# Optimization experiments

Measured on AMD Instinct MI355X. Metric: run time of the kernel, lower is better.

## Reference

```python
import jax, jax.numpy as jnp
import numpy as np

B, S, D, H = 8, 2048, 1024, 16
HD = D // H          # head_dim = 64
HID = 4 * HD         # hidden = 256
MAX_LR = 0.01
NUM_LAYERS = 2


def _split_heads(x):
    b, s, _ = x.shape
    return x.reshape(b, s, H, HD).transpose(0, 2, 1, 3).reshape(b * H, s, HD)


def _merge_heads(x, b):
    return x.reshape(b, H, -1, HD).transpose(0, 2, 1, 3).reshape(b, -1, D)


def _rmsnorm_w(x, w, eps=1e-6):
    # learned RMSNorm: x / rms(x) * w
    return x * w * jax.lax.rsqrt(jnp.mean(x * x, axis=-1, keepdims=True) + eps)


def _pf_rmsnorm(h):
    # parameter-free RMSNorm, returns (h_norm, rms)
    rms = jnp.sqrt(jnp.mean(h * h, axis=-1, keepdims=True) + 1e-8)
    return h / rms, rms


def _pf_rmsnorm_bwd(d_out, h_norm, rms):
    d = d_out.shape[-1]
    dy = jnp.sum(d_out * h_norm, axis=-1, keepdims=True)
    return (d_out - h_norm * dy / d) / rms


def _gelu_grad(x):
    cdf = 0.5 * (1.0 + jax.lax.erf(x * 0.7071067811865476))
    pdf = jnp.exp(-0.5 * x * x) * 0.3989422804014327
    return cdf + x * pdf


def _memory_forward(x, Ws):
    h = x
    n = len(Ws)
    for i, W in enumerate(Ws):
        h = jnp.matmul(h, W)  # (BH,S,din) @ (BH,din,dout)
        if i < n - 1:
            h = jax.nn.gelu(h, approximate=False)
    h = jnp.nan_to_num(h, nan=0.0, posinf=0.0, neginf=0.0)
    h_norm, _ = _pf_rmsnorm(h)
    return h_norm + x


def _memory_grad(keys, values, theta, Ws):
    Ws = [jax.lax.stop_gradient(W) for W in Ws]  # detach fast weights
    acts = [keys]
    pres = []
    h = keys
    n = len(Ws)
    for i, W in enumerate(Ws):
        pre = jnp.matmul(h, W)
        pres.append(pre)
        h = jax.nn.gelu(pre, approximate=False) if i < n - 1 else pre
        acts.append(h)
    h_norm, rms = _pf_rmsnorm(acts[-1])
    pred = h_norm + keys
    d_pred = 2.0 * theta[..., None] * (pred - values)
    d_h = _pf_rmsnorm_bwd(d_pred, h_norm, rms)
    grads = [None] * n
    for i in range(n - 1, -1, -1):
        grads[i] = jnp.einsum('bsi,bso->bio', acts[i], d_h)
        if i > 0:
            d_h = jnp.matmul(d_h, Ws[i].transpose(0, 2, 1)) * _gelu_grad(pres[i - 1])
    return grads


def _clip_grads(grads, max_norm=10.0):
    sq = sum(jnp.sum(g.reshape(g.shape[0], -1) ** 2, axis=1) for g in grads)
    coef = jnp.minimum(max_norm / (jnp.sqrt(sq) + 1e-6), 1.0)
    coef = jax.lax.stop_gradient(coef)[:, None, None]
    return [g * coef for g in grads]


def reference(x, W_K, W_V, W_Q, mem_W0, mem_W1, k_norm_w, q_norm_w,
              store_norm_w, retrieve_norm_w, alpha_w, alpha_b,
              theta_w, theta_b, eta_w, eta_b):
    b = x.shape[0]
    bh = b * H
    # init per-sample fast weights and zero momentum
    Ws = [jnp.broadcast_to(mem_W0, (bh,) + mem_W0.shape),
          jnp.broadcast_to(mem_W1, (bh,) + mem_W1.shape)]
    mom = [jnp.zeros_like(W) for W in Ws]
    # ---- update(x, ms, mom) ----
    x_n = _rmsnorm_w(x, store_norm_w)
    keys = _rmsnorm_w(_split_heads(x_n @ W_K), k_norm_w)
    values = _split_heads(x_n @ W_V)
    alpha = jax.nn.sigmoid(x_n @ alpha_w + alpha_b)          # (B,S,H)
    theta = jax.nn.sigmoid(x_n @ theta_w + theta_b) * MAX_LR
    eta = jax.nn.sigmoid(x_n @ eta_w + eta_b)
    to_bh = lambda t: t.transpose(0, 2, 1).reshape(bh, -1)   # (BH,S)
    alpha, theta, eta = to_bh(alpha), to_bh(theta), to_bh(eta)
    grads = _clip_grads(_memory_grad(keys, values, theta, Ws))
    a_mean = jnp.mean(alpha, axis=1)[:, None, None]
    e_mean = jnp.mean(eta, axis=1)[:, None, None]
    new_Ws = []
    for W, m, g in zip(Ws, mom, grads):
        new_m = e_mean * m - g
        new_w = (1.0 - a_mean) * W + new_m
        new_w = jnp.where(jnp.isfinite(new_w), new_w, jax.lax.stop_gradient(W))
        new_Ws.append(new_w)
    # ---- retrieve(x, new_ms) ----
    q = _rmsnorm_w(_split_heads(_rmsnorm_w(x, retrieve_norm_w) @ W_Q), q_norm_w)
    out = _memory_forward(q, new_Ws)
    return _merge_heads(out, b)


def setup_inputs() -> dict:
    key = jax.random.key(0)
    ks = jax.random.split(key, 12)
    xav0 = float(np.sqrt(2.0 / (HD + HID)))
    xav1 = float(np.sqrt(2.0 / (HID + HD)))
    return {
        'x': jax.random.normal(ks[0], (B, S, D), jnp.float32),
        'W_K': jax.random.normal(ks[1], (D, D), jnp.float32) / np.float32(np.sqrt(D)),
        'W_V': jax.random.normal(ks[2], (D, D), jnp.float32) / np.float32(np.sqrt(D)),
        'W_Q': jax.random.normal(ks[3], (D, D), jnp.float32) / np.float32(np.sqrt(D)),
        'mem_W0': jax.random.normal(ks[4], (HD, HID), jnp.float32) * xav0,
        'mem_W1': jax.random.normal(ks[5], (HID, HD), jnp.float32) * xav1,
        'k_norm_w': jnp.ones((HD,), jnp.float32),
        'q_norm_w': jnp.ones((HD,), jnp.float32),
        'store_norm_w': jnp.ones((D,), jnp.float32),
        'retrieve_norm_w': jnp.ones((D,), jnp.float32),
        'alpha_w': jax.random.normal(ks[6], (D, H), jnp.float32) * 0.01,
        'alpha_b': jnp.full((H,), -5.0, jnp.float32),
        'theta_w': jax.random.normal(ks[7], (D, H), jnp.float32) * 0.01,
        'theta_b': jnp.full((H,), -3.0, jnp.float32),
        'eta_w': jax.random.normal(ks[8], (D, H), jnp.float32) * 0.01,
        'eta_b': jnp.zeros((H,), jnp.float32),
    }
```

## Files before the change

### kernel.cpp

```cpp
#include <hip/hip_runtime.h>

typedef unsigned short u16;
typedef unsigned int   u32;

#define DEV static __device__ __forceinline__

constexpr int S    = 2048;
constexpr int D    = 1024;
constexpr int H    = 16;
constexpr int BB   = 8;
constexpr int BH   = BB * H;
constexpr int BS   = BB * S;
constexpr long NR  = (long)BH * S;
constexpr int GB   = 16;
constexpr int NG   = BH / GB;
constexpr int GR   = GB * S;

typedef __attribute__((ext_vector_type(8))) short bf16x8;
typedef __attribute__((ext_vector_type(4))) float f32x4;

DEV float b2f(u16 u) { return __uint_as_float(((u32)u) << 16); }
DEV u16   f2b(float f) {
  u32 x = __float_as_uint(f);
  u32 r = (x + 0x7fffu + ((x >> 16) & 1u)) >> 16;
  return (u16)r;
}
DEV float geluf(float x) { return 0.5f * x * (1.0f + erff(x * 0.70710678118654752440f)); }
DEV float sigmoidf(float z) { return 1.0f / (1.0f + expf(-z)); }
DEV float wsum(float v) {
#pragma unroll
  for (int o = 32; o > 0; o >>= 1) v += __shfl_xor(v, o, 64);
  return v;
}
DEV float rsum16(float v) {
  v += __shfl_xor(v, 1, 64);
  v += __shfl_xor(v, 2, 64);
  v += __shfl_xor(v, 4, 64);
  v += __shfl_xor(v, 8, 64);
  return v;
}
DEV float nan0(float v) {
  u32 b = __float_as_uint(v);
  return ((b & 0x7f800000u) == 0x7f800000u) ? 0.f : v;
}
DEV bool finitef(float v) {
  u32 b = __float_as_uint(v);
  return (b & 0x7f800000u) != 0x7f800000u;
}
DEV void dma16(const void* g, void* l) {
  __builtin_amdgcn_global_load_lds((const __attribute__((address_space(1))) void*)g,
                                   (__attribute__((address_space(3))) void*)l, 16, 0, 0);
}
DEV int swz4(int r) { return (r ^ (r >> 2)) & 3; }

template <bool FIRST>
__global__ void k_xnorm(const float* __restrict__ x, const float* __restrict__ cw,
                        float* __restrict__ rinv, u16* __restrict__ xb) {
  int row  = blockIdx.x * 4 + (threadIdx.x >> 6);
  int lane = threadIdx.x & 63;
  const float* p = x + (size_t)row * D;
  float4 v[4];
#pragma unroll
  for (int j = 0; j < 4; j++) v[j] = *(const float4*)(p + lane * 4 + j * 256);
  float rs;
  if (FIRST) {
    float s = 0.f;
#pragma unroll
    for (int j = 0; j < 4; j++)
      s += v[j].x * v[j].x + v[j].y * v[j].y + v[j].z * v[j].z + v[j].w * v[j].w;
    s = wsum(s);
    rs = rsqrtf(s * (1.0f / D) + 1e-6f);
    if (lane == 0) rinv[row] = rs;
  } else {
    rs = rinv[row];
  }
#pragma unroll
  for (int j = 0; j < 4; j++) {
    float4 w4 = *(const float4*)(cw + lane * 4 + j * 256);
    ushort4 o;
    o.x = f2b(v[j].x * rs * w4.x);
    o.y = f2b(v[j].y * rs * w4.y);
    o.z = f2b(v[j].z * rs * w4.z);
    o.w = f2b(v[j].w * rs * w4.w);
    *(ushort4*)&xb[(size_t)row * D + lane * 4 + j * 256] = o;
  }
}

__global__ void k_wtrans(const float* __restrict__ W0, const float* __restrict__ W1,
                         const float* __restrict__ W2, u16* __restrict__ WT) {
  __shared__ float tl[64][65];
  const float* W = blockIdx.z == 0 ? W0 : blockIdx.z == 1 ? W1 : W2;
  u16* dst = WT + (size_t)blockIdx.z * D * D;
  int bx = blockIdx.x, by = blockIdx.y;
  int t = threadIdx.x;
  int r = t >> 6, c = t & 63;
#pragma unroll
  for (int i = 0; i < 64; i += 4)
    tl[i + r][c] = W[(size_t)(bx * 64 + i + r) * D + by * 64 + c];
  __syncthreads();
// ... 129 lines not shown
    dma16(ga0 + k0 + 32, lA0h1);
    dma16(ga1 + k0 + 32, lA1h1);
    dma16(gb + k0, lB);
    __syncthreads();
#pragma unroll
    for (int h = 0; h < 2; h++) {
      bf16x8 af[2], bfr[2];
#pragma unroll
      for (int f = 0; f < 2; f++) {
        af[f]  = *(const bf16x8*)&As[h][aoff[f]];
        bfr[f] = *(const bf16x8*)&Bs[h][boff[f]];
      }
#pragma unroll
      for (int i = 0; i < 2; i++)
#pragma unroll
        for (int j = 0; j < 2; j++)
          acc[i][j] = __builtin_amdgcn_mfma_f32_16x16x32_bf16(af[i], bfr[j], acc[i][j], 0, 0, 0);
    }
    __syncthreads();
  }

#pragma unroll
  for (int fn = 0; fn < 2; fn++) {
    float bias = (fn == 0) ? ab[l15] : tb[l15];
    float scale = (fn == 0) ? 1.f : 0.01f;
    float* dst = (fn == 0) ? alpha : theta;
#pragma unroll
    for (int fm = 0; fm < 2; fm++) {
#pragma unroll
      for (int r = 0; r < 4; r++) {
        int gr = m0 + wave * 32 + fm * 16 + quad * 4 + r;
        int b = gr >> 11, s_ = gr & 2047;
        float v = sigmoidf(acc[fm][fn][r] + bias) * scale;
        dst[(long)(b * 16 + l15) * S + s_] = v;
      }
    }
  }
}

__global__ void k_mean(const float* __restrict__ alpha, float* __restrict__ amean) {
  int bh = blockIdx.x, t = threadIdx.x;
  float sa = 0.f;
  for (int i = t; i < S; i += 256) sa += alpha[(long)bh * S + i];
  sa = wsum(sa);
  __shared__ float sh[4];
  int w = t >> 6, lane = t & 63;
  if (lane == 0) sh[w] = sa;
  __syncthreads();
  if (t == 0) amean[bh] = (sh[0] + sh[1] + sh[2] + sh[3]) * (1.f / S);
}

__global__ void k_wsmall(const float* __restrict__ W0, const float* __restrict__ W1,
                         u16* __restrict__ W0T, u16* __restrict__ W1b, u16* __restrict__ W1T) {
  int idx = blockIdx.x * 256 + threadIdx.x;
  int sec = blockIdx.y;
  if (sec == 0) {
    int k = idx & 63, i = idx >> 6;
    W0T[idx] = f2b(W0[k * 256 + i]);
  } else if (sec == 1) {
    W1b[idx] = f2b(W1[idx]);
  } else {
    int i = idx & 255, o = idx >> 8;
    W1T[idx] = f2b(W1[i * 64 + o]);
  }
}

__global__ void k_keysT(const u16* __restrict__ keysg, u16* __restrict__ blk) {
  long idx = (long)blockIdx.x * 256 + threadIdx.x;
  int col = (int)(idx & 63);
  long s = (idx >> 6) * 4;
  ushort4 o;
  o.x = keysg[(size_t)s * 64 + col];
  o.y = keysg[(size_t)(s + 1) * 64 + col];
  o.z = keysg[(size_t)(s + 2) * 64 + col];
  o.w = keysg[(size_t)(s + 3) * 64 + col];
  *(ushort4*)&blk[((size_t)(s >> 4) * 4 + (col >> 4)) * 256 + (col & 15) * 16 + (s & 15)] = o;
}

__global__ __launch_bounds__(512, 2) void kfuse(
    const u16* __restrict__ keysv, const u16* __restrict__ vals,
    const u16* __restrict__ keysTb,
    const u16* __restrict__ W0T, const u16* __restrict__ W1T,
    const u16* __restrict__ W1b, const float* __restrict__ theta,
    float* __restrict__ g0t, float* __restrict__ g1t) {
  __shared__ u16 L[57344];
  u16* S1   = L;
  u16* W0sL = L + 32768;
  u16* dhR  = L + 32768;
  u16* dhblk = L + 40960;
  u16* Kblk = L + 49152;

  int t = threadIdx.x;
  int w = t >> 6, lane = t & 63;
  int quad = lane >> 4, l15 = lane & 15;
  int bh = blockIdx.y, strip = blockIdx.x;
  long grow = (long)bh * S + strip * 128;
  int bswz = (quad ^ swz4(l15)) * 8;

  {
    const u16* ksrc = keysTb + (grow >> 4) * 1024 + (size_t)w * 1024 + lane * 8;
    dma16(ksrc, Kblk + w * 1024);
    dma16(ksrc + 512, Kblk + w * 1024 + 512);
    int i = t >> 1, c = t & 1;
    int key = swz4(i & 15);
    const u16* gsrc = W0T + i * 64 + c * 32;
    u16* ldst = W0sL + c * 8192 + i * 32;
#pragma unroll
    for (int j = 0; j < 4; j++)
      *(bf16x8*)&ldst[j * 8] = *(const bf16x8*)&gsrc[(j ^ key) * 8];
  }
  __syncthreads();

  f32x4 acc2[4];
  ushort4 gpr[16];
  {
    f32x4 acc[16] = {};
    bf16x8 afA[2];
#pragma unroll
    for (int kc = 0; kc < 2; kc++) {
      union { bf16x8 v; u16 e[8]; } u;
#pragma unroll
      for (int j = 0; j < 8; j++) {
        int k = kc * 32 + quad * 8 + j;
        u.e[j] = Kblk[(w * 4 + (k >> 4)) * 256 + (k & 15) * 16 + l15];
      }
      afA[kc] = u.v;
    }
#pragma unroll
    for (int f = 0; f < 16; f++) {
      bf16x8 b0 = *(const bf16x8*)&W0sL[(f * 16 + l15) * 32 + bswz];
      bf16x8 b1 = *(const bf16x8*)&W0sL[8192 + (f * 16 + l15) * 32 + bswz];
      acc[f] = __builtin_amdgcn_mfma_f32_16x16x32_bf16(afA[0], b0, acc[f], 0, 0, 0);
      acc[f] = __builtin_amdgcn_mfma_f32_16x16x32_bf16(afA[1], b1, acc[f], 0, 0, 0);
    }
    __syncthreads();

#pragma unroll
    for (int f = 0; f < 16; f++) {
      ushort4 oa, og;
#pragma unroll
      for (int r = 0; r < 4; r++) {
        float v = acc[f][r];
        float cdf = 0.5f * (1.0f + erff(v * 0.70710678118654752440f));
        float pdf = expf(-0.5f * v * v) * 0.3989422804014327f;
        ((u16*)&oa)[r] = f2b(v * cdf);
        ((u16*)&og)[r] = f2b(cdf + v * pdf);
      }
      *(ushort4*)&S1[(w * 16 + f) * 256 + l15 * 16 + quad * 4] = oa;
      gpr[f] = og;
    }
  }

  {
#pragma unroll
    for (int fn = 0; fn < 4; fn++) acc2[fn] = (f32x4){};
#pragma unroll
    for (int kc = 0; kc < 8; kc++) {
      union { bf16x8 v; u16 e[8]; } u;
#pragma unroll
      for (int j = 0; j < 8; j++) {
        int c = kc * 32 + quad * 8 + j;
        u.e[j] = S1[(w * 16 + (c >> 4)) * 256 + (c & 15) * 16 + l15];
      }
#pragma unroll
      for (int fn = 0; fn < 4; fn++) {
        bf16x8 bv = *(const bf16x8*)&W1T[(size_t)(fn * 16 + l15) * 256 + kc * 32 + quad * 8];
        acc2[fn] = __builtin_amdgcn_mfma_f32_16x16x32_bf16(u.v, bv, acc2[fn], 0, 0, 0);
      }
    }
  }

  {
    f32x4 ss = acc2[0] * acc2[0] + acc2[1] * acc2[1] +
               acc2[2] * acc2[2] + acc2[3] * acc2[3];
    f32x4 rrms, th2;
    long rowg0 = grow + w * 16 + quad * 4;
#pragma unroll
    for (int r = 0; r < 4; r++) {
      float s = rsum16(ss[r]);
      rrms[r] = rsqrtf(s * (1.f / 64) + 1e-8f);
      th2[r] = 2.f * theta[rowg0 + r];
    }
    f32x4 hn[4], dp[4];
    f32x4 dyp = {};
#pragma unroll
    for (int fn = 0; fn < 4; fn++) {
      int col = fn * 16 + l15;
#pragma unroll
      for (int r = 0; r < 4; r++) {
        float h = acc2[fn][r] * rrms[r];
        float k = b2f(keysv[(rowg0 + r) * 64 + col]);
        float v = b2f(vals[(rowg0 + r) * 64 + col]);
        float d = th2[r] * (h + k - v);
        hn[fn][r] = h;
        dp[fn][r] = d;
        dyp[r] += d * h;
      }
    }
#pragma unroll
    for (int r = 0; r < 4; r++) dyp[r] = rsum16(dyp[r]);
#pragma unroll
    for (int fn = 0; fn < 4; fn++) {
      int col = fn * 16 + l15;
      ushort4 ob;
#pragma unroll
      for (int r = 0; r < 4; r++) {
        float d = (dp[fn][r] - hn[fn][r] * dyp[r] * (1.f / 64)) * rrms[r];
        u16 db = f2b(d);
        ((u16*)&ob)[r] = db;
        int row = w * 16 + quad * 4 + r;
        int g = ((col >> 3) & 3) ^ swz4(row & 15);
        dhR[(col >> 5) * 4096 + row * 32 + g * 8 + (col & 7)] = db;
      }
      *(ushort4*)&dhblk[(w * 4 + fn) * 256 + l15 * 16 + quad * 4] = ob;
    }
  }
  __syncthreads();

  {
    int qh = quad >> 1, ql = (quad & 1) * 8;
    f32x4 a3[4][2] = {};
#pragma unroll
    for (int ks = 0; ks < 4; ks++) {
      int s16 = ks * 2 + qh;
      bf16x8 af[4], bf2[2];
#pragma unroll
      for (int m = 0; m < 4; m++)
        af[m] = *(const bf16x8*)&dhblk[(s16 * 4 + m) * 256 + l15 * 16 + ql];
#pragma unroll
      for (int f2 = 0; f2 < 2; f2++)
        bf2[f2] = *(const bf16x8*)&S1[(s16 * 16 + w * 2 + f2) * 256 + l15 * 16 + ql];
#pragma unroll
      for (int m = 0; m < 4; m++)
#pragma unroll
        for (int f2 = 0; f2 < 2; f2++)
          a3[m][f2] = __builtin_amdgcn_mfma_f32_16x16x32_bf16(af[m], bf2[f2], a3[m][f2], 0, 0, 0);
    }
    float* gp1 = g1t + (size_t)bh * 16384;
#pragma unroll
    for (int m = 0; m < 4; m++)
#pragma unroll
      for (int f2 = 0; f2 < 2; f2++) {
        int n = w * 32 + f2 * 16 + l15;
#pragma unroll
        for (int r = 0; r < 4; r++)
          atomicAdd(&gp1[(size_t)(m * 16 + quad * 4 + r) * 256 + n], a3[m][f2][r]);
      }
  }
  __syncthreads();

  {
    f32x4 a5[16] = {};
    bf16x8 afd[2];
#pragma unroll
    for (int kc = 0; kc < 2; kc++)
      afd[kc] = *(const bf16x8*)&dhR[kc * 4096 + (w * 16 + l15) * 32 + bswz];
#pragma unroll
    for (int f = 0; f < 16; f++) {
#pragma unroll
      for (int kc = 0; kc < 2; kc++) {
        bf16x8 bv = *(const bf16x8*)&W1b[(size_t)(f * 16 + l15) * 64 + kc * 32 + quad * 8];
        a5[f] = __builtin_amdgcn_mfma_f32_16x16x32_bf16(afd[kc], bv, a5[f], 0, 0, 0);
      }
    }
#pragma unroll
    for (int f = 0; f < 16; f++) {
      ushort4 od;
#pragma unroll
      for (int r = 0; r < 4; r++)
        ((u16*)&od)[r] = f2b(a5[f][r] * b2f(((u16*)&gpr[f])[r]));
      *(ushort4*)&S1[(w * 16 + f) * 256 + l15 * 16 + quad * 4] = od;
    }
  }
  __syncthreads();

  {
    int qh = quad >> 1, ql = (quad & 1) * 8;
    f32x4 a6[4][2] = {};
#pragma unroll
    for (int ks = 0; ks < 4; ks++) {
      int s16 = ks * 2 + qh;
      bf16x8 af[4], bf2[2];
#pragma unroll
      for (int m = 0; m < 4; m++)
        af[m] = *(const bf16x8*)&Kblk[(s16 * 4 + m) * 256 + l15 * 16 + ql];
#pragma unroll
      for (int f2 = 0; f2 < 2; f2++)
        bf2[f2] = *(const bf16x8*)&S1[(s16 * 16 + w * 2 + f2) * 256 + l15 * 16 + ql];
#pragma unroll
      for (int m = 0; m < 4; m++)
#pragma unroll
        for (int f2 = 0; f2 < 2; f2++)
          a6[m][f2] = __builtin_amdgcn_mfma_f32_16x16x32_bf16(af[m], bf2[f2], a6[m][f2], 0, 0, 0);
    }
    float* gp0 = g0t + (size_t)bh * 16384;
#pragma unroll
    for (int m = 0; m < 4; m++)
#pragma unroll
      for (int f2 = 0; f2 < 2; f2++) {
        int n = w * 32 + f2 * 16 + l15;
#pragma unroll
        for (int r = 0; r < 4; r++)
          atomicAdd(&gp0[(size_t)(m * 16 + quad * 4 + r) * 256 + n], a6[m][f2][r]);
      }
  }
}

__global__ __launch_bounds__(256) void km64r(
    const u16* __restrict__ A, const u16* __restrict__ BT, long bstride,
    u16* __restrict__ o_act) {
  __shared__ u16 As[128 * 32];
  __shared__ u16 Bs[128 * 32];
  int t = threadIdx.x;
  int wave = t >> 6, lane = t & 63;
  int wm = wave >> 1, wn = wave & 1;
  long rowbase = (long)blockIdx.z * S + (long)blockIdx.y * 128;
  int n0 = blockIdx.x * 128;
  int quad = lane >> 4, l15 = lane & 15;
  int rl = lane >> 2;
  int q = (lane & 3) ^ swz4(rl);
  const u16* Bp = BT + (long)blockIdx.z * bstride;

  f32x4 acc[4][4] = {};
  int aoff[4], boff[4];
#pragma unroll
  for (int f = 0; f < 4; f++) {
    aoff[f] = (wm * 64 + f * 16 + l15) * 32 + (quad ^ swz4(l15)) * 8;
    boff[f] = (wn * 64 + f * 16 + l15) * 32 + (quad ^ swz4(l15)) * 8;
  }
  const u16* ga0 = A + (rowbase + wave * 32 + rl) * 64 + q * 8;
  const u16* ga1 = ga0 + 16 * 64;
  const u16* gb0 = Bp + (size_t)(n0 + wave * 32 + rl) * 64 + q * 8;
  const u16* gb1 = gb0 + 16 * 64;
  u16* lA0 = &As[(wave * 32) * 32];
  u16* lA1 = &As[(wave * 32 + 16) * 32];
  u16* lB0 = &Bs[(wave * 32) * 32];
  u16* lB1 = &Bs[(wave * 32 + 16) * 32];

  for (int k0 = 0; k0 < 64; k0 += 32) {
    dma16(ga0 + k0, lA0);
    dma16(ga1 + k0, lA1);
    dma16(gb0 + k0, lB0);
    dma16(gb1 + k0, lB1);
    __syncthreads();
    bf16x8 af[4], bfr[4];
#pragma unroll
    for (int f = 0; f < 4; f++) {
      af[f]  = *(const bf16x8*)&As[aoff[f]];
      bfr[f] = *(const bf16x8*)&Bs[boff[f]];
    }
#pragma unroll
    for (int i = 0; i < 4; i++)
#pragma unroll
      for (int j = 0; j < 4; j++)
        acc[i][j] = __builtin_amdgcn_mfma_f32_16x16x32_bf16(af[i], bfr[j], acc[i][j], 0, 0, 0);
    __syncthreads();
  }

#pragma unroll
  for (int fm = 0; fm < 4; fm++) {
    long sbase = rowbase + wm * 64 + fm * 16;
#pragma unroll
    for (int fn = 0; fn < 4; fn++) {
      int col = n0 + wn * 64 + fn * 16 + l15;
#pragma unroll
      for (int r = 0; r < 4; r++) {
        long row = sbase + quad * 4 + r;
        o_act[row * 256 + col] = f2b(geluf(acc[fm][fn][r]));
      }
    }
  }
}

__global__ __launch_bounds__(256) void km256r(
    const u16* __restrict__ A, const u16* __restrict__ BT, long bstride,
    const u16* __restrict__ qp, long grow0, float* __restrict__ outp) {
  __shared__ u16 As[256 * 32];
  __shared__ u16 Bs[64 * 32];
  int t = threadIdx.x;
  int wave = t >> 6, lane = t & 63;
  long rowbase = (long)blockIdx.z * S + (long)blockIdx.y * 256;
  int quad = lane >> 4, l15 = lane & 15;
  int rl = lane >> 2;
  int q = (lane & 3) ^ swz4(rl);
  const u16* Bp = BT + (long)blockIdx.z * bstride;

  f32x4 acc[4][4] = {};
  int aoff[4], boff[4];
#pragma unroll
  for (int f = 0; f < 4; f++) {
    aoff[f] = (wave * 64 + f * 16 + l15) * 32 + (quad ^ swz4(l15)) * 8;
    boff[f] = (f * 16 + l15) * 32 + (quad ^ swz4(l15)) * 8;
  }
  const u16* ga = A + (rowbase + wave * 64 + rl) * 256 + q * 8;
  const u16* gb = Bp + (size_t)(wave * 16 + rl) * 256 + q * 8;
  u16* lA0 = &As[(wave * 64) * 32];
  u16* lA1 = &As[(wave * 64 + 16) * 32];
  u16* lA2 = &As[(wave * 64 + 32) * 32];
  u16* lA3 = &As[(wave * 64 + 48) * 32];
  u16* lB  = &Bs[(wave * 16) * 32];

  for (int k0 = 0; k0 < 256; k0 += 32) {
    dma16(ga + k0, lA0);
    dma16(ga + 16 * 256 + k0, lA1);
    dma16(ga + 32 * 256 + k0, lA2);
    dma16(ga + 48 * 256 + k0, lA3);
    dma16(gb + k0, lB);
    __syncthreads();
    bf16x8 af[4], bfr[4];
#pragma unroll
    for (int f = 0; f < 4; f++) {
      af[f]  = *(const bf16x8*)&As[aoff[f]];
      bfr[f] = *(const bf16x8*)&Bs[boff[f]];
    }
#pragma unroll
    for (int i = 0; i < 4; i++)
#pragma unroll
      for (int j = 0; j < 4; j++)
        acc[i][j] = __builtin_amdgcn_mfma_f32_16x16x32_bf16(af[i], bfr[j], acc[i][j], 0, 0, 0);
    __syncthreads();
  }

#pragma unroll
  for (int fm = 0; fm < 4; fm++) {
    long sbase = rowbase + wave * 64 + fm * 16;
    f32x4 hv[4];
    f32x4 ss = {};
#pragma unroll
    for (int fn = 0; fn < 4; fn++) {
#pragma unroll
      for (int r = 0; r < 4; r++) {
        float v = nan0(acc[fm][fn][r]);
        hv[fn][r] = v;
        ss[r] += v * v;
      }
    }
    f32x4 rrms;
#pragma unroll
    for (int r = 0; r < 4; r++) {
      float s = rsum16(ss[r]);
      rrms[r] = rsqrtf(s * (1.f / 64) + 1e-8f);
    }
#pragma unroll
    for (int r = 0; r < 4; r++) {
      long gr = grow0 + sbase + quad * 4 + r;
      long bhn = gr >> 11, s_ = gr & 2047;
      long b = bhn >> 4, hh = bhn & 15;
      size_t obase = (size_t)(b * S + s_) * D + hh * 64;
#pragma unroll
      for (int fn = 0; fn < 4; fn++) {
        int col = fn * 16 + l15;
        outp[obase + col] = hv[fn][r] * rrms[r] + b2f(qp[gr * 64 + col]);
      }
    }
  }
}

__global__ void k_zero(float* __restrict__ p, long n) {
  long i = (long)blockIdx.x * 256 + threadIdx.x;
  if (i < n) p[i] = 0.f;
}

__global__ void k_clip(const float* __restrict__ g0, const float* __restrict__ g1,
                       float* __restrict__ coef) {
  int bh = blockIdx.x, t = threadIdx.x;
  const float* p0 = g0 + (long)bh * 16384;
  const float* p1 = g1 + (long)bh * 16384;
  float s = 0.f;
  for (int i = t; i < 16384; i += 256) {
    float a = p0[i]; s += a * a;
    float b = p1[i]; s += b * b;
  }
  s = wsum(s);
  __shared__ float sh[4];
  int w = t >> 6, lane = t & 63;
  if (lane == 0) sh[w] = s;
  __syncthreads();
  if (t == 0) {
    float tot = sh[0] + sh[1] + sh[2] + sh[3];
    float c = 10.f / (sqrtf(tot) + 1e-6f);
    coef[bh] = fminf(c, 1.f);
  }
}

__global__ void k_updT(const float* __restrict__ W0, const float* __restrict__ W1,
                       const float* __restrict__ g0t, const float* __restrict__ g1t,
                       const float* __restrict__ amean, const float* __restrict__ coef,
                       u16* __restrict__ nW0T, u16* __restrict__ nW1T) {
  long i = (long)blockIdx.x * 256 + threadIdx.x;
  int half = (int)(i >> 21);
  long j = i & ((1L << 21) - 1);
  int bh = (int)(j >> 14);
  int idx = (int)(j & 16383);
  float a = 1.f - amean[bh], cf = coef[bh];
  if (half == 0) {
    int k = idx & 63, ii = idx >> 6;
    float w = W0[k * 256 + ii];
    float nw = a * w - cf * g0t[(long)bh * 16384 + k * 256 + ii];
    if (!finitef(nw)) nw = w;
    nW0T[j] = f2b(nw);
  } else {
    int ii = idx & 255, o = idx >> 8;
    float w = W1[ii * 64 + o];
    float nw = a * w - cf * g1t[(long)bh * 16384 + idx];
    if (!finitef(nw)) nw = w;
    nW1T[j] = f2b(nw);
  }
}

extern "C" void kernel_launch(void* const* d_in, const int* in_sizes, int n_in,
                              void* d_out, int out_size, void* d_ws, size_t ws_size,
                              hipStream_t stream) {
  const float* x   = (const float*)d_in[0];
  const float* W_K = (const float*)d_in[1];
  const float* W_V = (const float*)d_in[2];
  const float* W_Q = (const float*)d_in[3];
  const float* mW0 = (const float*)d_in[4];
  const float* mW1 = (const float*)d_in[5];
  const float* knw = (const float*)d_in[6];
  const float* qnw = (const float*)d_in[7];
  const float* snw = (const float*)d_in[8];
  const float* rnw = (const float*)d_in[9];
  const float* aw  = (const float*)d_in[10];
  const float* ab  = (const float*)d_in[11];
  const float* tw  = (const float*)d_in[12];
  const float* tb  = (const float*)d_in[13];
  float* out = (float*)d_out;
  (void)ws_size; (void)in_sizes; (void)n_in; (void)out_size;

  char* w = (char*)d_ws;
  auto alloc = [&](size_t bytes) {
    char* p = w;
    w += (bytes + 255) / 256 * 256;
    return p;
  };
  float* rinv   = (float*)alloc((size_t)BS * 4);
  u16*   xs     = (u16*)alloc((size_t)BS * D * 2);
  u16*   WTb    = (u16*)alloc((size_t)3 * D * D * 2);
  u16*   keys   = (u16*)alloc(NR * 64 * 2);
  u16*   vals   = (u16*)alloc(NR * 64 * 2);
  float* alpha  = (float*)alloc(NR * 4);
  float* theta  = (float*)alloc(NR * 4);
  float* amean  = (float*)alloc(BH * 4);
  float* coef   = (float*)alloc(BH * 4);
  u16*   W0T    = (u16*)alloc(16384 * 2);
  u16*   W1b    = (u16*)alloc(16384 * 2);
  u16*   W1T    = (u16*)alloc(16384 * 2);
  u16*   atw    = (u16*)alloc((size_t)32 * D * 2);
  u16*   keysTb = (u16*)alloc(NR * 64 * 2);
  u16*   act0   = (u16*)alloc((size_t)GR * 256 * 2);
  float* g0t    = (float*)alloc((size_t)BH * 16384 * 4);
  float* g1t    = (float*)alloc((size_t)BH * 16384 * 4);
  u16*   nW0T   = (u16*)alloc((size_t)BH * 16384 * 2);
  u16*   nW1T   = (u16*)alloc((size_t)BH * 16384 * 2);

  k_xnorm<true><<<BS / 4, 256, 0, stream>>>(x, snw, rinv, xs);
  k_wtrans<<<dim3(16, 16, 3), 256, 0, stream>>>(W_K, W_V, W_Q, WTb);
  k_atw<<<128, 256, 0, stream>>>(aw, tw, atw);
  k_proj_mfma<true><<<dim3(8, 128), 256, 0, stream>>>(xs, WTb, knw, keys);
  k_proj_mfma<false><<<dim3(8, 128), 256, 0, stream>>>(xs, WTb + (size_t)D * D, nullptr, vals);
  k_ate2<<<BS / 128, 256, 0, stream>>>(xs, atw, ab, tb, alpha, theta);
  k_mean<<<BH, 256, 0, stream>>>(alpha, amean);
  k_wsmall<<<dim3(64, 3), 256, 0, stream>>>(mW0, mW1, W0T, W1b, W1T);
  k_zero<<<(int)((2L * BH * 16384 + 255) / 256), 256, 0, stream>>>(g0t, 2L * BH * 16384);

  k_keysT<<<(int)(NR / 16), 256, 0, stream>>>(keys, keysTb);
  kfuse<<<dim3(16, BH), 512, 0, stream>>>(keys, vals, keysTb, W0T, W1T, W1b,
                                          theta, g0t, g1t);

  k_clip<<<BH, 256, 0, stream>>>(g0t, g1t, coef);
  k_updT<<<(int)(2L * BH * 16384 / 256), 256, 0, stream>>>(
      mW0, mW1, g0t, g1t, amean, coef, nW0T, nW1T);

  k_xnorm<false><<<BS / 4, 256, 0, stream>>>(x, rnw, rinv, xs);
  u16* q = keys;
  k_proj_mfma<true><<<dim3(8, 128), 256, 0, stream>>>(xs, WTb + (size_t)2 * D * D, qnw, q);
  for (int g = 0; g < NG; g++) {
    long bh0 = (long)g * GB;
    long grow0 = bh0 * S;
    km64r<<<dim3(2, S / 128, GB), 256, 0, stream>>>(
        q + grow0 * 64, nW0T + bh0 * 16384, 16384, act0);
    km256r<<<dim3(1, S / 256, GB), 256, 0, stream>>>(
        act0, nW1T + bh0 * 16384, 16384, q, grow0, out);
  }
}
```

Measured before the change: 980.3 us.

## Accumulate memory gradients in registers across strips, drop atomics and zeroing

```diff
diff --git a/kernel.cpp b/kernel.cpp
--- a/kernel.cpp
+++ b/kernel.cpp
@@ -310,25 +310,25 @@
     const u16* __restrict__ keysTb,
     const u16* __restrict__ W0T, const u16* __restrict__ W1T,
     const u16* __restrict__ W1b, const float* __restrict__ theta,
-    float* __restrict__ g0t, float* __restrict__ g1t) {
-  __shared__ u16 L[57344];
-  u16* S1   = L;
-  u16* W0sL = L + 32768;
-  u16* dhR  = L + 32768;
-  u16* dhblk = L + 40960;
-  u16* Kblk = L + 49152;
+    float* __restrict__ g0p, float* __restrict__ g1p) {
+  __shared__ u16 L[73728];
+  u16* S1    = L;
+  u16* W0sL  = L + 32768;
+  u16* dhR   = L + 49152;
+  u16* dhblk = L + 57344;
+  u16* Kblk  = L + 65536;
 
   int t = threadIdx.x;
   int w = t >> 6, lane = t & 63;
   int quad = lane >> 4, l15 = lane & 15;
-  int bh = blockIdx.y, strip = blockIdx.x;
-  long grow = (long)bh * S + strip * 128;
+  int bh = blockIdx.y, half = blockIdx.x;
   int bswz = (quad ^ swz4(l15)) * 8;
+  int qh = quad >> 1, ql = (quad & 1) * 8;
+
+  f32x4 g1a[4][2] = {};
+  f32x4 g0a[4][2] = {};
 
   {
-    const u16* ksrc = keysTb + (grow >> 4) * 1024 + (size_t)w * 1024 + lane * 8;
-    dma16(ksrc, Kblk + w * 1024);
-    dma16(ksrc + 512, Kblk + w * 1024 + 512);
     int i = t >> 1, c = t & 1;
     int key = swz4(i & 15);
     const u16* gsrc = W0T + i * 64 + c * 32;
@@ -337,201 +337,202 @@
     for (int j = 0; j < 4; j++)
       *(bf16x8*)&ldst[j * 8] = *(const bf16x8*)&gsrc[(j ^ key) * 8];
   }
-  __syncthreads();
-
-  f32x4 acc2[4];
-  ushort4 gpr[16];
-  {
-    f32x4 acc[16] = {};
-    bf16x8 afA[2];
-#pragma unroll
-    for (int kc = 0; kc < 2; kc++) {
-      union { bf16x8 v; u16 e[8]; } u;
-#pragma unroll
-      for (int j = 0; j < 8; j++) {
-        int k = kc * 32 + quad * 8 + j;
-        u.e[j] = Kblk[(w * 4 + (k >> 4)) * 256 + (k & 15) * 16 + l15];
-      }
-      afA[kc] = u.v;
-    }
-#pragma unroll
-    for (int f = 0; f < 16; f++) {
-      bf16x8 b0 = *(const bf16x8*)&W0sL[(f * 16 + l15) * 32 + bswz];
-      bf16x8 b1 = *(const bf16x8*)&W0sL[8192 + (f * 16 + l15) * 32 + bswz];
-      acc[f] = __builtin_amdgcn_mfma_f32_16x16x32_bf16(afA[0], b0, acc[f], 0, 0, 0);
-      acc[f] = __builtin_amdgcn_mfma_f32_16x16x32_bf16(afA[1], b1, acc[f], 0, 0, 0);
-    }
-    __syncthreads();
-
-#pragma unroll
-    for (int f = 0; f < 16; f++) {
-      ushort4 oa, og;
+
+  for (int strip = half * 8; strip < half * 8 + 8; ++strip) {
+    long grow = (long)bh * S + strip * 128;
+
+    {
+      const u16* ksrc = keysTb + (grow >> 4) * 1024 + (size_t)w * 1024 + lane * 8;
+      dma16(ksrc, Kblk + w * 1024);
+      dma16(ksrc + 512, Kblk + w * 1024 + 512);
+    }
+    __syncthreads();
+
+    f32x4 acc2[4];
+    ushort4 gpr[16];
+    {
+      f32x4 acc[16] = {};
+      bf16x8 afA[2];
+#pragma unroll
+      for (int kc = 0; kc < 2; kc++) {
+        union { bf16x8 v; u16 e[8]; } u;
+#pragma unroll
+        for (int j = 0; j < 8; j++) {
+          int k = kc * 32 + quad * 8 + j;
+          u.e[j] = Kblk[(w * 4 + (k >> 4)) * 256 + (k & 15) * 16 + l15];
+        }
+        afA[kc] = u.v;
+      }
+#pragma unroll
+      for (int f = 0; f < 16; f++) {
+        bf16x8 b0 = *(const bf16x8*)&W0sL[(f * 16 + l15) * 32 + bswz];
+        bf16x8 b1 = *(const bf16x8*)&W0sL[8192 + (f * 16 + l15) * 32 + bswz];
+        acc[f] = __builtin_amdgcn_mfma_f32_16x16x32_bf16(afA[0], b0, acc[f], 0, 0, 0);
+        acc[f] = __builtin_amdgcn_mfma_f32_16x16x32_bf16(afA[1], b1, acc[f], 0, 0, 0);
+      }
+
+#pragma unroll
+      for (int f = 0; f < 16; f++) {
+        ushort4 oa, og;
+#pragma unroll
+        for (int r = 0; r < 4; r++) {
+          float v = acc[f][r];
+          float cdf = 0.5f * (1.0f + erff(v * 0.70710678118654752440f));
+          float pdf = expf(-0.5f * v * v) * 0.3989422804014327f;
+          ((u16*)&oa)[r] = f2b(v * cdf);
+          ((u16*)&og)[r] = f2b(cdf + v * pdf);
+        }
+        *(ushort4*)&S1[(w * 16 + f) * 256 + l15 * 16 + quad * 4] = oa;
+        gpr[f] = og;
+      }
+    }
+
+    {
+#pragma unroll
+      for (int fn = 0; fn < 4; fn++) acc2[fn] = (f32x4){};
+#pragma unroll
+      for (int kc = 0; kc < 8; kc++) {
+        union { bf16x8 v; u16 e[8]; } u;
+#pragma unroll
+        for (int j = 0; j < 8; j++) {
+          int c = kc * 32 + quad * 8 + j;
+          u.e[j] = S1[(w * 16 + (c >> 4)) * 256 + (c & 15) * 16 + l15];
+        }
+#pragma unroll
+        for (int fn = 0; fn < 4; fn++) {
+          bf16x8 bv = *(const bf16x8*)&W1T[(size_t)(fn * 16 + l15) * 256 + kc * 32 + quad * 8];
+          acc2[fn] = __builtin_amdgcn_mfma_f32_16x16x32_bf16(u.v, bv, acc2[fn], 0, 0, 0);
+        }
+      }
+    }
+
+    {
+      f32x4 ss = acc2[0] * acc2[0] + acc2[1] * acc2[1] +
+                 acc2[2] * acc2[2] + acc2[3] * acc2[3];
+      f32x4 rrms, th2;
+      long rowg0 = grow + w * 16 + quad * 4;
 #pragma unroll
       for (int r = 0; r < 4; r++) {
-        float v = acc[f][r];
-        float cdf = 0.5f * (1.0f + erff(v * 0.70710678118654752440f));
-        float pdf = expf(-0.5f * v * v) * 0.3989422804014327f;
-        ((u16*)&oa)[r] = f2b(v * cdf);
-        ((u16*)&og)[r] = f2b(cdf + v * pdf);
-      }
-      *(ushort4*)&S1[(w * 16 + f) * 256 + l15 * 16 + quad * 4] = oa;
-      gpr[f] = og;
-    }
-  }
-
-  {
-#pragma unroll
-    for (int fn = 0; fn < 4; fn++) acc2[fn] = (f32x4){};
-#pragma unroll
-    for (int kc = 0; kc < 8; kc++) {
-      union { bf16x8 v; u16 e[8]; } u;
-#pragma unroll
-      for (int j = 0; j < 8; j++) {
-        int c = kc * 32 + quad * 8 + j;
-        u.e[j] = S1[(w * 16 + (c >> 4)) * 256 + (c & 15) * 16 + l15];
-      }
+        float s = rsum16(ss[r]);
+        rrms[r] = rsqrtf(s * (1.f / 64) + 1e-8f);
+        th2[r] = 2.f * theta[rowg0 + r];
+      }
+      f32x4 hn[4], dp[4];
+      f32x4 dyp = {};
 #pragma unroll
       for (int fn = 0; fn < 4; fn++) {
-        bf16x8 bv = *(const bf16x8*)&W1T[(size_t)(fn * 16 + l15) * 256 + kc * 32 + quad * 8];
-        acc2[fn] = __builtin_amdgcn_mfma_f32_16x16x32_bf16(u.v, bv, acc2[fn], 0, 0, 0);
-      }
-    }
-  }
-
-  {
-    f32x4 ss = acc2[0] * acc2[0] + acc2[1] * acc2[1] +
-               acc2[2] * acc2[2] + acc2[3] * acc2[3];
-    f32x4 rrms, th2;
-    long rowg0 = grow + w * 16 + quad * 4;
-#pragma unroll
-    for (int r = 0; r < 4; r++) {
-      float s = rsum16(ss[r]);
-      rrms[r] = rsqrtf(s * (1.f / 64) + 1e-8f);
-      th2[r] = 2.f * theta[rowg0 + r];
-    }
-    f32x4 hn[4], dp[4];
-    f32x4 dyp = {};
-#pragma unroll
-    for (int fn = 0; fn < 4; fn++) {
-      int col = fn * 16 + l15;
+        int col = fn * 16 + l15;
+#pragma unroll
+        for (int r = 0; r < 4; r++) {
+          float h = acc2[fn][r] * rrms[r];
+          float k = b2f(keysv[(rowg0 + r) * 64 + col]);
+          float v = b2f(vals[(rowg0 + r) * 64 + col]);
+          float d = th2[r] * (h + k - v);
+          hn[fn][r] = h;
+          dp[fn][r] = d;
+          dyp[r] += d * h;
+        }
+      }
+#pragma unroll
+      for (int r = 0; r < 4; r++) dyp[r] = rsum16(dyp[r]);
+#pragma unroll
+      for (int fn = 0; fn < 4; fn++) {
+        int col = fn * 16 + l15;
+        ushort4 ob;
+#pragma unroll
+        for (int r = 0; r < 4; r++) {
+          float d = (dp[fn][r] - hn[fn][r] * dyp[r] * (1.f / 64)) * rrms[r];
+          u16 db = f2b(d);
+          ((u16*)&ob)[r] = db;
+          int row = w * 16 + quad * 4 + r;
+          int g = ((col >> 3) & 3) ^ swz4(row & 15);
+          dhR[(col >> 5) * 4096 + row * 32 + g * 8 + (col & 7)] = db;
+        }
+        *(ushort4*)&dhblk[(w * 4 + fn) * 256 + l15 * 16 + quad * 4] = ob;
+      }
+    }
+    __syncthreads();
+
+    {
+#pragma unroll
+      for (int ks = 0; ks < 4; ks++) {
+        int s16 = ks * 2 + qh;
+        bf16x8 af[4], bf2[2];
+#pragma unroll
+        for (int m = 0; m < 4; m++)
+          af[m] = *(const bf16x8*)&dhblk[(s16 * 4 + m) * 256 + l15 * 16 + ql];
+#pragma unroll
+        for (int f2 = 0; f2 < 2; f2++)
+          bf2[f2] = *(const bf16x8*)&S1[(s16 * 16 + w * 2 + f2) * 256 + l15 * 16 + ql];
+#pragma unroll
+        for (int m = 0; m < 4; m++)
+#pragma unroll
+          for (int f2 = 0; f2 < 2; f2++)
+            g1a[m][f2] = __builtin_amdgcn_mfma_f32_16x16x32_bf16(af[m], bf2[f2], g1a[m][f2], 0, 0, 0);
+      }
+    }
+    __syncthreads();
+
+    {
+      f32x4 a5[16] = {};
+      bf16x8 afd[2];
+#pragma unroll
+      for (int kc = 0; kc < 2; kc++)
+        afd[kc] = *(const bf16x8*)&dhR[kc * 4096 + (w * 16 + l15) * 32 + bswz];
+#pragma unroll
+      for (int f = 0; f < 16; f++) {
+#pragma unroll
+        for (int kc = 0; kc < 2; kc++) {
+          bf16x8 bv = *(const bf16x8*)&W1b[(size_t)(f * 16 + l15) * 64 + kc * 32 + quad * 8];
+          a5[f] = __builtin_amdgcn_mfma_f32_16x16x32_bf16(afd[kc], bv, a5[f], 0, 0, 0);
+        }
+      }
+#pragma unroll
+      for (int f = 0; f < 16; f++) {
+        ushort4 od;
+#pragma unroll
+        for (int r = 0; r < 4; r++)
+          ((u16*)&od)[r] = f2b(a5[f][r] * b2f(((u16*)&gpr[f])[r]));
+        *(ushort4*)&S1[(w * 16 + f) * 256 + l15 * 16 + quad * 4] = od;
+      }
+    }
+    __syncthreads();
+
+    {
+#pragma unroll
+      for (int ks = 0; ks < 4; ks++) {
+        int s16 = ks * 2 + qh;
+        bf16x8 af[4], bf2[2];
+#pragma unroll
+        for (int m = 0; m < 4; m++)
+          af[m] = *(const bf16x8*)&Kblk[(s16 * 4 + m) * 256 + l15 * 16 + ql];
+#pragma unroll
+        for (int f2 = 0; f2 < 2; f2++)
+          bf2[f2] = *(const bf16x8*)&S1[(s16 * 16 + w * 2 + f2) * 256 + l15 * 16 + ql];
+#pragma unroll
+        for (int m = 0; m < 4; m++)
+#pragma unroll
+          for (int f2 = 0; f2 < 2; f2++)
+            g0a[m][f2] = __builtin_amdgcn_mfma_f32_16x16x32_bf16(af[m], bf2[f2], g0a[m][f2], 0, 0, 0);
+      }
+    }
+    __syncthreads();
+  }
+
+  float* gp1 = g1p + ((size_t)half * BH + bh) * 16384;
+  float* gp0 = g0p + ((size_t)half * BH + bh) * 16384;
+#pragma unroll
+  for (int m = 0; m < 4; m++)
+#pragma unroll
+    for (int f2 = 0; f2 < 2; f2++) {
+      int n = w * 32 + f2 * 16 + l15;
 #pragma unroll
       for (int r = 0; r < 4; r++) {
-        float h = acc2[fn][r] * rrms[r];
-        float k = b2f(keysv[(rowg0 + r) * 64 + col]);
-        float v = b2f(vals[(rowg0 + r) * 64 + col]);
-        float d = th2[r] * (h + k - v);
-        hn[fn][r] = h;
-        dp[fn][r] = d;
-        dyp[r] += d * h;
-      }
-    }
-#pragma unroll
-    for (int r = 0; r < 4; r++) dyp[r] = rsum16(dyp[r]);
-#pragma unroll
-    for (int fn = 0; fn < 4; fn++) {
-      int col = fn * 16 + l15;
-      ushort4 ob;
-#pragma unroll
-      for (int r = 0; r < 4; r++) {
-        float d = (dp[fn][r] - hn[fn][r] * dyp[r] * (1.f / 64)) * rrms[r];
-        u16 db = f2b(d);
-        ((u16*)&ob)[r] = db;
-        int row = w * 16 + quad * 4 + r;
-        int g = ((col >> 3) & 3) ^ swz4(row & 15);
-        dhR[(col >> 5) * 4096 + row * 32 + g * 8 + (col & 7)] = db;
-      }
-      *(ushort4*)&dhblk[(w * 4 + fn) * 256 + l15 * 16 + quad * 4] = ob;
-    }
-  }
-  __syncthreads();
-
-  {
-    int qh = quad >> 1, ql = (quad & 1) * 8;
-    f32x4 a3[4][2] = {};
-#pragma unroll
-    for (int ks = 0; ks < 4; ks++) {
-      int s16 = ks * 2 + qh;
-      bf16x8 af[4], bf2[2];
-#pragma unroll
-      for (int m = 0; m < 4; m++)
-        af[m] = *(const bf16x8*)&dhblk[(s16 * 4 + m) * 256 + l15 * 16 + ql];
-#pragma unroll
-      for (int f2 = 0; f2 < 2; f2++)
-        bf2[f2] = *(const bf16x8*)&S1[(s16 * 16 + w * 2 + f2) * 256 + l15 * 16 + ql];
-#pragma unroll
-      for (int m = 0; m < 4; m++)
-#pragma unroll
-        for (int f2 = 0; f2 < 2; f2++)
-          a3[m][f2] = __builtin_amdgcn_mfma_f32_16x16x32_bf16(af[m], bf2[f2], a3[m][f2], 0, 0, 0);
-    }
-    float* gp1 = g1t + (size_t)bh * 16384;
-#pragma unroll
-    for (int m = 0; m < 4; m++)
-#pragma unroll
-      for (int f2 = 0; f2 < 2; f2++) {
-        int n = w * 32 + f2 * 16 + l15;
-#pragma unroll
-        for (int r = 0; r < 4; r++)
-          atomicAdd(&gp1[(size_t)(m * 16 + quad * 4 + r) * 256 + n], a3[m][f2][r]);
-      }
-  }
-  __syncthreads();
-
-  {
-    f32x4 a5[16] = {};
-    bf16x8 afd[2];
-#pragma unroll
-    for (int kc = 0; kc < 2; kc++)
-      afd[kc] = *(const bf16x8*)&dhR[kc * 4096 + (w * 16 + l15) * 32 + bswz];
-#pragma unroll
-    for (int f = 0; f < 16; f++) {
-#pragma unroll
-      for (int kc = 0; kc < 2; kc++) {
-        bf16x8 bv = *(const bf16x8*)&W1b[(size_t)(f * 16 + l15) * 64 + kc * 32 + quad * 8];
-        a5[f] = __builtin_amdgcn_mfma_f32_16x16x32_bf16(afd[kc], bv, a5[f], 0, 0, 0);
-      }
-    }
-#pragma unroll
-    for (int f = 0; f < 16; f++) {
-      ushort4 od;
-#pragma unroll
-      for (int r = 0; r < 4; r++)
-        ((u16*)&od)[r] = f2b(a5[f][r] * b2f(((u16*)&gpr[f])[r]));
-      *(ushort4*)&S1[(w * 16 + f) * 256 + l15 * 16 + quad * 4] = od;
-    }
-  }
-  __syncthreads();
-
-  {
-    int qh = quad >> 1, ql = (quad & 1) * 8;
-    f32x4 a6[4][2] = {};
-#pragma unroll
-    for (int ks = 0; ks < 4; ks++) {
-      int s16 = ks * 2 + qh;
-      bf16x8 af[4], bf2[2];
-#pragma unroll
-      for (int m = 0; m < 4; m++)
-        af[m] = *(const bf16x8*)&Kblk[(s16 * 4 + m) * 256 + l15 * 16 + ql];
-#pragma unroll
-      for (int f2 = 0; f2 < 2; f2++)
-        bf2[f2] = *(const bf16x8*)&S1[(s16 * 16 + w * 2 + f2) * 256 + l15 * 16 + ql];
-#pragma unroll
-      for (int m = 0; m < 4; m++)
-#pragma unroll
-        for (int f2 = 0; f2 < 2; f2++)
-          a6[m][f2] = __builtin_amdgcn_mfma_f32_16x16x32_bf16(af[m], bf2[f2], a6[m][f2], 0, 0, 0);
-    }
-    float* gp0 = g0t + (size_t)bh * 16384;
-#pragma unroll
-    for (int m = 0; m < 4; m++)
-#pragma unroll
-      for (int f2 = 0; f2 < 2; f2++) {
-        int n = w * 32 + f2 * 16 + l15;
-#pragma unroll
-        for (int r = 0; r < 4; r++)
-          atomicAdd(&gp0[(size_t)(m * 16 + quad * 4 + r) * 256 + n], a6[m][f2][r]);
-      }
-  }
+        size_t off = (size_t)(m * 16 + quad * 4 + r) * 256 + n;
+        gp1[off] = g1a[m][f2][r];
+        gp0[off] = g0a[m][f2][r];
+      }
+    }
 }
 
 __global__ __launch_bounds__(256) void km64r(
@@ -684,20 +685,16 @@
   }
 }
 
-__global__ void k_zero(float* __restrict__ p, long n) {
-  long i = (long)blockIdx.x * 256 + threadIdx.x;
-  if (i < n) p[i] = 0.f;
-}
-
-__global__ void k_clip(const float* __restrict__ g0, const float* __restrict__ g1,
+__global__ void k_clip(const float* __restrict__ g0p, const float* __restrict__ g1p,
                        float* __restrict__ coef) {
   int bh = blockIdx.x, t = threadIdx.x;
-  const float* p0 = g0 + (long)bh * 16384;
-  const float* p1 = g1 + (long)bh * 16384;
+  const long HS = (long)BH * 16384;
+  const float* p0 = g0p + (long)bh * 16384;
+  const float* p1 = g1p + (long)bh * 16384;
   float s = 0.f;
   for (int i = t; i < 16384; i += 256) {
-    float a = p0[i]; s += a * a;
-    float b = p1[i]; s += b * b;
+    float a = p0[i] + p0[HS + i]; s += a * a;
+    float b = p1[i] + p1[HS + i]; s += b * b;
   }
   s = wsum(s);
   __shared__ float sh[4];
@@ -712,7 +709,7 @@
 }
 
 __global__ void k_updT(const float* __restrict__ W0, const float* __restrict__ W1,
-                       const float* __restrict__ g0t, const float* __restrict__ g1t,
+                       const float* __restrict__ g0p, const float* __restrict__ g1p,
                        const float* __restrict__ amean, const float* __restrict__ coef,
                        u16* __restrict__ nW0T, u16* __restrict__ nW1T) {
   long i = (long)blockIdx.x * 256 + threadIdx.x;
@@ -720,17 +717,20 @@
   long j = i & ((1L << 21) - 1);
   int bh = (int)(j >> 14);
   int idx = (int)(j & 16383);
+  const long HS = (long)BH * 16384;
   float a = 1.f - amean[bh], cf = coef[bh];
   if (half == 0) {
     int k = idx & 63, ii = idx >> 6;
     float w = W0[k * 256 + ii];
-    float nw = a * w - cf * g0t[(long)bh * 16384 + k * 256 + ii];
+    long o = (long)bh * 16384 + k * 256 + ii;
+    float nw = a * w - cf * (g0p[o] + g0p[HS + o]);
     if (!finitef(nw)) nw = w;
     nW0T[j] = f2b(nw);
   } else {
-    int ii = idx & 255, o = idx >> 8;
-    float w = W1[ii * 64 + o];
-    float nw = a * w - cf * g1t[(long)bh * 16384 + idx];
+    int ii = idx & 255, o2 = idx >> 8;
+    float w = W1[ii * 64 + o2];
+    long o = (long)bh * 16384 + idx;
+    float nw = a * w - cf * (g1p[o] + g1p[HS + o]);
     if (!finitef(nw)) nw = w;
     nW1T[j] = f2b(nw);
   }
@@ -777,8 +777,8 @@
   u16*   atw    = (u16*)alloc((size_t)32 * D * 2);
   u16*   keysTb = (u16*)alloc(NR * 64 * 2);
   u16*   act0   = (u16*)alloc((size_t)GR * 256 * 2);
-  float* g0t    = (float*)alloc((size_t)BH * 16384 * 4);
-  float* g1t    = (float*)alloc((size_t)BH * 16384 * 4);
+  float* g0p    = (float*)alloc((size_t)2 * BH * 16384 * 4);
+  float* g1p    = (float*)alloc((size_t)2 * BH * 16384 * 4);
   u16*   nW0T   = (u16*)alloc((size_t)BH * 16384 * 2);
   u16*   nW1T   = (u16*)alloc((size_t)BH * 16384 * 2);
 
@@ -790,15 +790,14 @@
   k_ate2<<<BS / 128, 256, 0, stream>>>(xs, atw, ab, tb, alpha, theta);
   k_mean<<<BH, 256, 0, stream>>>(alpha, amean);
   k_wsmall<<<dim3(64, 3), 256, 0, stream>>>(mW0, mW1, W0T, W1b, W1T);
-  k_zero<<<(int)((2L * BH * 16384 + 255) / 256), 256, 0, stream>>>(g0t, 2L * BH * 16384);
 
   k_keysT<<<(int)(NR / 16), 256, 0, stream>>>(keys, keysTb);
-  kfuse<<<dim3(16, BH), 512, 0, stream>>>(keys, vals, keysTb, W0T, W1T, W1b,
-                                          theta, g0t, g1t);
-
-  k_clip<<<BH, 256, 0, stream>>>(g0t, g1t, coef);
+  kfuse<<<dim3(2, BH), 512, 0, stream>>>(keys, vals, keysTb, W0T, W1T, W1b,
+                                         theta, g0p, g1p);
+
+  k_clip<<<BH, 256, 0, stream>>>(g0p, g1p, coef);
   k_updT<<<(int)(2L * BH * 16384 / 256), 256, 0, stream>>>(
-      mW0, mW1, g0t, g1t, amean, coef, nW0T, nW1T);
+      mW0, mW1, g0p, g1p, amean, coef, nW0T, nW1T);
 
   k_xnorm<false><<<BS / 4, 256, 0, stream>>>(x, rnw, rinv, xs);
   u16* q = keys;
```

Measured after the change: 1.014 ms. 3.4% more time.

## Fuse two-layer memory retrieval MLP into one kernel keeping hidden activations in LDS

Applied to the files above, without the earlier changes.

```diff
diff --git a/kernel.cpp b/kernel.cpp
--- a/kernel.cpp
+++ b/kernel.cpp
@@ -12,9 +12,6 @@
 constexpr int BH   = BB * H;
 constexpr int BS   = BB * S;
 constexpr long NR  = (long)BH * S;
-constexpr int GB   = 16;
-constexpr int NG   = BH / GB;
-constexpr int GR   = GB * S;
 
 typedef __attribute__((ext_vector_type(8))) short bf16x8;
 typedef __attribute__((ext_vector_type(4))) float f32x4;
@@ -534,131 +531,92 @@
   }
 }
 
-__global__ __launch_bounds__(256) void km64r(
-    const u16* __restrict__ A, const u16* __restrict__ BT, long bstride,
-    u16* __restrict__ o_act) {
-  __shared__ u16 As[128 * 32];
-  __shared__ u16 Bs[128 * 32];
+__global__ __launch_bounds__(512, 2) void kret(
+    const u16* __restrict__ qp, const u16* __restrict__ qTb,
+    const u16* __restrict__ nW0T, const u16* __restrict__ nW1T,
+    float* __restrict__ outp) {
+  __shared__ u16 L[57344];
+  u16* S1   = L;
+  u16* W0sL = L + 32768;
+  u16* Kblk = L + 49152;
+
   int t = threadIdx.x;
-  int wave = t >> 6, lane = t & 63;
-  int wm = wave >> 1, wn = wave & 1;
-  long rowbase = (long)blockIdx.z * S + (long)blockIdx.y * 128;
-  int n0 = blockIdx.x * 128;
+  int w = t >> 6, lane = t & 63;
   int quad = lane >> 4, l15 = lane & 15;
-  int rl = lane >> 2;
-  int q = (lane & 3) ^ swz4(rl);
-  const u16* Bp = BT + (long)blockIdx.z * bstride;
-
-  f32x4 acc[4][4] = {};
-  int aoff[4], boff[4];
-#pragma unroll
-  for (int f = 0; f < 4; f++) {
-    aoff[f] = (wm * 64 + f * 16 + l15) * 32 + (quad ^ swz4(l15)) * 8;
-    boff[f] = (wn * 64 + f * 16 + l15) * 32 + (quad ^ swz4(l15)) * 8;
-  }
-  const u16* ga0 = A + (rowbase + wave * 32 + rl) * 64 + q * 8;
-  const u16* ga1 = ga0 + 16 * 64;
-  const u16* gb0 = Bp + (size_t)(n0 + wave * 32 + rl) * 64 + q * 8;
-  const u16* gb1 = gb0 + 16 * 64;
-  u16* lA0 = &As[(wave * 32) * 32];
-  u16* lA1 = &As[(wave * 32 + 16) * 32];
-  u16* lB0 = &Bs[(wave * 32) * 32];
-  u16* lB1 = &Bs[(wave * 32 + 16) * 32];
-
-  for (int k0 = 0; k0 < 64; k0 += 32) {
-    dma16(ga0 + k0, lA0);
-    dma16(ga1 + k0, lA1);
-    dma16(gb0 + k0, lB0);
-    dma16(gb1 + k0, lB1);
-    __syncthreads();
-    bf16x8 af[4], bfr[4];
-#pragma unroll
-    for (int f = 0; f < 4; f++) {
-      af[f]  = *(const bf16x8*)&As[aoff[f]];
-      bfr[f] = *(const bf16x8*)&Bs[boff[f]];
-    }
-#pragma unroll
-    for (int i = 0; i < 4; i++)
-#pragma unroll
-      for (int j = 0; j < 4; j++)
-        acc[i][j] = __builtin_amdgcn_mfma_f32_16x16x32_bf16(af[i], bfr[j], acc[i][j], 0, 0, 0);
-    __syncthreads();
-  }
-
-#pragma unroll
-  for (int fm = 0; fm < 4; fm++) {
-    long sbase = rowbase + wm * 64 + fm * 16;
+  int bh = blockIdx.y, strip = blockIdx.x;
+  long grow = (long)bh * S + strip * 128;
+  int bswz = (quad ^ swz4(l15)) * 8;
+
+  {
+    const u16* ksrc = qTb + (grow >> 4) * 1024 + (size_t)w * 1024 + lane * 8;
+    dma16(ksrc, Kblk + w * 1024);
+    dma16(ksrc + 512, Kblk + w * 1024 + 512);
+    int i = t >> 1, c = t & 1;
+    int key = swz4(i & 15);
+    const u16* gsrc = nW0T + (size_t)bh * 16384 + i * 64 + c * 32;
+    u16* ldst = W0sL + c * 8192 + i * 32;
+#pragma unroll
+    for (int j = 0; j < 4; j++)
+      *(bf16x8*)&ldst[j * 8] = *(const bf16x8*)&gsrc[(j ^ key) * 8];
+  }
+  __syncthreads();
+
+  {
+    f32x4 acc[16] = {};
+    bf16x8 afA[2];
+#pragma unroll
+    for (int kc = 0; kc < 2; kc++) {
+      union { bf16x8 v; u16 e[8]; } u;
+#pragma unroll
+      for (int j = 0; j < 8; j++) {
+        int k = kc * 32 + quad * 8 + j;
+        u.e[j] = Kblk[(w * 4 + (k >> 4)) * 256 + (k & 15) * 16 + l15];
+      }
+      afA[kc] = u.v;
+    }
+#pragma unroll
+    for (int f = 0; f < 16; f++) {
+      bf16x8 b0 = *(const bf16x8*)&W0sL[(f * 16 + l15) * 32 + bswz];
+      bf16x8 b1 = *(const bf16x8*)&W0sL[8192 + (f * 16 + l15) * 32 + bswz];
+      acc[f] = __builtin_amdgcn_mfma_f32_16x16x32_bf16(afA[0], b0, acc[f], 0, 0, 0);
+      acc[f] = __builtin_amdgcn_mfma_f32_16x16x32_bf16(afA[1], b1, acc[f], 0, 0, 0);
+    }
+#pragma unroll
+    for (int f = 0; f < 16; f++) {
+      ushort4 oa;
+#pragma unroll
+      for (int r = 0; r < 4; r++) ((u16*)&oa)[r] = f2b(geluf(acc[f][r]));
+      *(ushort4*)&S1[(w * 16 + f) * 256 + l15 * 16 + quad * 4] = oa;
+    }
+  }
+
+  f32x4 acc2[4];
+#pragma unroll
+  for (int fn = 0; fn < 4; fn++) acc2[fn] = (f32x4){};
+  const u16* W1p = nW1T + (size_t)bh * 16384;
+#pragma unroll
+  for (int kc = 0; kc < 8; kc++) {
+    union { bf16x8 v; u16 e[8]; } u;
+#pragma unroll
+    for (int j = 0; j < 8; j++) {
+      int c = kc * 32 + quad * 8 + j;
+      u.e[j] = S1[(w * 16 + (c >> 4)) * 256 + (c & 15) * 16 + l15];
+    }
 #pragma unroll
     for (int fn = 0; fn < 4; fn++) {
-      int col = n0 + wn * 64 + fn * 16 + l15;
-#pragma unroll
-      for (int r = 0; r < 4; r++) {
-        long row = sbase + quad * 4 + r;
-        o_act[row * 256 + col] = f2b(geluf(acc[fm][fn][r]));
-      }
-    }
-  }
-}
-
-__global__ __launch_bounds__(256) void km256r(
-    const u16* __restrict__ A, const u16* __restrict__ BT, long bstride,
-    const u16* __restrict__ qp, long grow0, float* __restrict__ outp) {
-  __shared__ u16 As[256 * 32];
-  __shared__ u16 Bs[64 * 32];
-  int t = threadIdx.x;
-  int wave = t >> 6, lane = t & 63;
-  long rowbase = (long)blockIdx.z * S + (long)blockIdx.y * 256;
-  int quad = lane >> 4, l15 = lane & 15;
-  int rl = lane >> 2;
-  int q = (lane & 3) ^ swz4(rl);
-  const u16* Bp = BT + (long)blockIdx.z * bstride;
-
-  f32x4 acc[4][4] = {};
-  int aoff[4], boff[4];
-#pragma unroll
-  for (int f = 0; f < 4; f++) {
-    aoff[f] = (wave * 64 + f * 16 + l15) * 32 + (quad ^ swz4(l15)) * 8;
-    boff[f] = (f * 16 + l15) * 32 + (quad ^ swz4(l15)) * 8;
-  }
-  const u16* ga = A + (rowbase + wave * 64 + rl) * 256 + q * 8;
-  const u16* gb = Bp + (size_t)(wave * 16 + rl) * 256 + q * 8;
-  u16* lA0 = &As[(wave * 64) * 32];
-  u16* lA1 = &As[(wave * 64 + 16) * 32];
-  u16* lA2 = &As[(wave * 64 + 32) * 32];
-  u16* lA3 = &As[(wave * 64 + 48) * 32];
-  u16* lB  = &Bs[(wave * 16) * 32];
-
-  for (int k0 = 0; k0 < 256; k0 += 32) {
-    dma16(ga + k0, lA0);
-    dma16(ga + 16 * 256 + k0, lA1);
-    dma16(ga + 32 * 256 + k0, lA2);
-    dma16(ga + 48 * 256 + k0, lA3);
-    dma16(gb + k0, lB);
-    __syncthreads();
-    bf16x8 af[4], bfr[4];
-#pragma unroll
-    for (int f = 0; f < 4; f++) {
-      af[f]  = *(const bf16x8*)&As[aoff[f]];
-      bfr[f] = *(const bf16x8*)&Bs[boff[f]];
-    }
-#pragma unroll
-    for (int i = 0; i < 4; i++)
-#pragma unroll
-      for (int j = 0; j < 4; j++)
-        acc[i][j] = __builtin_amdgcn_mfma_f32_16x16x32_bf16(af[i], bfr[j], acc[i][j], 0, 0, 0);
-    __syncthreads();
-  }
-
-#pragma unroll
-  for (int fm = 0; fm < 4; fm++) {
-    long sbase = rowbase + wave * 64 + fm * 16;
+      bf16x8 bv = *(const bf16x8*)&W1p[(size_t)(fn * 16 + l15) * 256 + kc * 32 + quad * 8];
+      acc2[fn] = __builtin_amdgcn_mfma_f32_16x16x32_bf16(u.v, bv, acc2[fn], 0, 0, 0);
+    }
+  }
+
+  {
     f32x4 hv[4];
     f32x4 ss = {};
 #pragma unroll
     for (int fn = 0; fn < 4; fn++) {
 #pragma unroll
       for (int r = 0; r < 4; r++) {
-        float v = nan0(acc[fm][fn][r]);
+        float v = nan0(acc2[fn][r]);
         hv[fn][r] = v;
         ss[r] += v * v;
       }
@@ -669,11 +627,11 @@
       float s = rsum16(ss[r]);
       rrms[r] = rsqrtf(s * (1.f / 64) + 1e-8f);
     }
+    long b = bh >> 4, hh = bh & 15;
 #pragma unroll
     for (int r = 0; r < 4; r++) {
-      long gr = grow0 + sbase + quad * 4 + r;
-      long bhn = gr >> 11, s_ = gr & 2047;
-      long b = bhn >> 4, hh = bhn & 15;
+      long s_ = strip * 128 + w * 16 + quad * 4 + r;
+      long gr = grow + w * 16 + quad * 4 + r;
       size_t obase = (size_t)(b * S + s_) * D + hh * 64;
 #pragma unroll
       for (int fn = 0; fn < 4; fn++) {
@@ -776,7 +734,6 @@
   u16*   W1T    = (u16*)alloc(16384 * 2);
   u16*   atw    = (u16*)alloc((size_t)32 * D * 2);
   u16*   keysTb = (u16*)alloc(NR * 64 * 2);
-  u16*   act0   = (u16*)alloc((size_t)GR * 256 * 2);
   float* g0t    = (float*)alloc((size_t)BH * 16384 * 4);
   float* g1t    = (float*)alloc((size_t)BH * 16384 * 4);
   u16*   nW0T   = (u16*)alloc((size_t)BH * 16384 * 2);
@@ -803,12 +760,6 @@
   k_xnorm<false><<<BS / 4, 256, 0, stream>>>(x, rnw, rinv, xs);
   u16* q = keys;
   k_proj_mfma<true><<<dim3(8, 128), 256, 0, stream>>>(xs, WTb + (size_t)2 * D * D, qnw, q);
-  for (int g = 0; g < NG; g++) {
-    long bh0 = (long)g * GB;
-    long grow0 = bh0 * S;
-    km64r<<<dim3(2, S / 128, GB), 256, 0, stream>>>(
-        q + grow0 * 64, nW0T + bh0 * 16384, 16384, act0);
-    km256r<<<dim3(1, S / 256, GB), 256, 0, stream>>>(
-        act0, nW1T + bh0 * 16384, 16384, q, grow0, out);
-  }
-}
+  k_keysT<<<(int)(NR / 16), 256, 0, stream>>>(q, keysTb);
+  kret<<<dim3(16, BH), 512, 0, stream>>>(q, keysTb, nW0T, nW1T, out);
+}
```

Result: faster. 899.7 us (-8.2%).
